# Optimization experiments

Hardware: AMD Instinct MI355X
Metric: run time of the kernel (lower is better)

Reference implementation:

```python
import jax, jax.numpy as jnp
import numpy as np

B, P, M, C = 128, 8732, 16, 3
THRESHOLD, NEG_POS_RATIO, ALPHA = 0.5, 3, 1.0


def xy_to_cxcy(xy):
    return jnp.concatenate([(xy[..., 2:] + xy[..., :2]) / 2.0, xy[..., 2:] - xy[..., :2]], axis=-1)


def cxcy_to_xy(cxcy):
    return jnp.concatenate([cxcy[..., :2] - cxcy[..., 2:] / 2.0, cxcy[..., :2] + cxcy[..., 2:] / 2.0], axis=-1)


def cxcy_to_gcxgcy(cxcy, priors_cxcy):
    return jnp.concatenate([
        (cxcy[..., :2] - priors_cxcy[..., :2]) / (priors_cxcy[..., 2:] / 10.0),
        jnp.log(cxcy[..., 2:] / priors_cxcy[..., 2:]) * 5.0], axis=-1)


def jaccard(a, b):
    # a: (M,4) xyxy, b: (P,4) xyxy -> (M,P) IoU
    lt = jnp.maximum(a[:, None, :2], b[None, :, :2])
    rb = jnp.minimum(a[:, None, 2:], b[None, :, 2:])
    wh = jnp.clip(rb - lt, 0.0)
    inter = wh[..., 0] * wh[..., 1]
    area_a = (a[:, 2] - a[:, 0]) * (a[:, 3] - a[:, 1])
    area_b = (b[:, 2] - b[:, 0]) * (b[:, 3] - b[:, 1])
    return inter / (area_a[:, None] + area_b[None, :] - inter)


def setup_inputs() -> dict:
    key = jax.random.key(0)
    k1, k2, k3, k4, k5, k6 = jax.random.split(key, 6)
    predicted_locs = jax.random.normal(k1, (B, P, 4), dtype=jnp.float32)
    predicted_scores = jax.random.normal(k2, (B, P, C), dtype=jnp.float32)
    xy = jax.random.uniform(k3, (B, M, 2), minval=0.0, maxval=0.7)
    wh = jax.random.uniform(k4, (B, M, 2), minval=0.05, maxval=0.3)
    boxes = jnp.concatenate([xy, xy + wh], axis=-1).astype(jnp.float32)
    labels = jax.random.randint(k5, (B, M), 1, 4)  # classes {1,2,3}
    pc = jax.random.uniform(k6, (P, 2), minval=0.0, maxval=1.0)
    pwh = jax.random.uniform(jax.random.fold_in(k6, 1), (P, 2), minval=0.05, maxval=0.5)
    priors_cxcy = jnp.concatenate([pc, pwh], axis=-1).astype(jnp.float32)
    return {"predicted_locs": predicted_locs, "predicted_scores": predicted_scores,
            "boxes": boxes, "labels": labels, "priors_cxcy": priors_cxcy}


def _match_one(boxes_i, labels_i, priors_xy, priors_cxcy):
    ov = jaccard(boxes_i, priors_xy)                # (M, P)
    ov_prior = ov.max(axis=0)                       # best overlap per prior
    obj_prior = ov.argmax(axis=0)                   # best object per prior
    prior_obj = ov.argmax(axis=1)                   # best prior per object
    n_obj = boxes_i.shape[0]
    obj_prior = obj_prior.at[prior_obj].set(jnp.arange(n_obj))
    ov_prior = ov_prior.at[prior_obj].set(1.0)
    lab = jnp.where(ov_prior < THRESHOLD, 0, labels_i[obj_prior])
    tl = cxcy_to_gcxgcy(xy_to_cxcy(boxes_i[obj_prior]), priors_cxcy)
    return tl, lab


def reference(predicted_locs, predicted_scores, boxes, labels, priors_cxcy):
    priors_xy = cxcy_to_xy(priors_cxcy)
    true_locs, true_classes = jax.vmap(_match_one, in_axes=(0, 0, None, None))(
        boxes, labels, priors_xy, priors_cxcy)      # (B,P,4), (B,P)
    positive = true_classes > 0                      # (B,P)
    n_pos = positive.sum(axis=1)                     # (B,)
    n_pos_total = n_pos.sum()

    # localization loss: L1Loss (mean over selected positive elements)
    l1 = jnp.abs(predicted_locs - true_locs).sum(axis=-1)   # (B,P)
    loc_loss = jnp.where(n_pos_total > 0,
                         (l1 * positive).sum() / (4.0 * jnp.maximum(n_pos_total, 1).astype(jnp.float32)),
                         0.0)

    # multi-label one-hot targets (classes 1,2,3; 3 = pair -> targets cols 1&2)
    tc = true_classes.reshape(-1)
    ignore = tc == -1
    pair = tc == 3
    target = jax.nn.one_hot(tc + 1, 5, dtype=predicted_scores.dtype)[:, 1:4]  # (B*P,3)
    target = target.at[:, 1].set(jnp.where(pair, 1.0, target[:, 1]))
    target = target.at[:, 2].set(jnp.where(pair, 1.0, target[:, 2]))

    # BCEWithLogits, summed over classes
    logits = predicted_scores.reshape(-1, C)
    bce = (jnp.logaddexp(0.0, logits) - logits * target).sum(axis=1)  # (B*P,)
    conf_all = jnp.where(ignore, 0.0, bce).reshape(true_classes.shape)  # (B,P)

    conf_pos = (conf_all * positive).sum()
    conf_neg = jnp.where(positive, 0.0, conf_all)
    conf_neg_sorted = -jnp.sort(-conf_neg, axis=1)   # descending per row
    ranks = jnp.arange(P)[None, :]
    hard_neg = ranks < (NEG_POS_RATIO * n_pos)[:, None]
    conf_hard_neg = (conf_neg_sorted * hard_neg).sum()

    conf_loss = (conf_hard_neg + conf_pos) / (1e-10 + n_pos_total.astype(jnp.float32))
    total = conf_loss + ALPHA * loc_loss
    return total, conf_loss, loc_loss, n_pos
```

## Files before the change

### kernel.cpp

```cpp
#include <hip/hip_runtime.h>
#include <hip/hip_fp16.h>
#include <cstdint>
#include <cmath>

#define B_ 128
#define P_ 8732
#define QU_ 2183
#define M_ 16
#define NT 1024
#define NW 16
#define NP9 9
#define TAIL_ (QU_ - 2*NT)

__device__ __forceinline__ float softplusf(float x) {
    float e = __builtin_amdgcn_exp2f(fabsf(x) * -1.44269504f);
    return fmaxf(x, 0.0f) + 0.69314718f * __builtin_amdgcn_logf(1.0f + e);
}

__device__ __forceinline__ float wred_sum_f(float v) {
#pragma unroll
    for (int o = 32; o > 0; o >>= 1) v += __shfl_down(v, o, 64);
    return v;
}
__device__ __forceinline__ int wred_sum_i(int v) {
#pragma unroll
    for (int o = 32; o > 0; o >>= 1) v += __shfl_down(v, o, 64);
    return v;
}

__device__ __forceinline__ void phaseD(
    int r, int p, float bv, int bm, float4 pr,
    float x0, float x1, float x2,
    const float* s_boxes, const int* s_labels,
    const float* __restrict__ plocs,
    unsigned char* __restrict__ objov, unsigned short* __restrict__ bcew,
    int& np, float& cp, float& ls)
{
    bool pos = bv >= 0.5f;
    objov[(size_t)r * P_ + p] = (unsigned char)(bm | (pos ? 0x80 : 0));
    int lab = pos ? s_labels[bm] : 0;
    float t0 = (lab == 0) ? 1.0f : 0.0f;
    float t1 = (lab == 1 || lab == 3) ? 1.0f : 0.0f;
    float t2 = (lab == 2 || lab == 3) ? 1.0f : 0.0f;
    float bce = (softplusf(x0) - x0*t0) + (softplusf(x1) - x1*t1) + (softplusf(x2) - x2*t2);
    float hb = 0.0f;
    if (pos) {
        np++; cp += bce;
        float4 bb = ((const float4*)s_boxes)[bm];
        float cx = (bb.x + bb.z) * 0.5f, cy = (bb.y + bb.w) * 0.5f;
        float w = bb.z - bb.x, hh = bb.w - bb.y;
        float g0 = (cx - pr.x) / (pr.z * 0.1f);
        float g1 = (cy - pr.y) / (pr.w * 0.1f);
        float g2 = logf(w / pr.z) * 5.0f;
        float g3 = logf(hh / pr.w) * 5.0f;
        float4 pl = ((const float4*)plocs)[(size_t)r * P_ + p];
        ls += fabsf(pl.x - g0) + fabsf(pl.y - g1) + fabsf(pl.z - g2) + fabsf(pl.w - g3);
    } else {
        hb = bce;
    }
    bcew[(size_t)r * P_ + p] = __half_as_ushort(__float2half(hb));
}

__global__ __launch_bounds__(NT) void mbox_match_kernel(
    const float* __restrict__ plocs,
    const float* __restrict__ pscores,
    const float* __restrict__ boxes,
    const int*   __restrict__ labels,
    const float* __restrict__ priors,
    unsigned char* __restrict__ objov,
    unsigned short* __restrict__ bcew,
    int2* __restrict__ cand,
    float* __restrict__ pcf, float* __restrict__ plc, int* __restrict__ pnp,
    unsigned int* __restrict__ gz)
{
    __shared__ float s_boxes[M_ * 4];
    __shared__ float s_area[M_];
    __shared__ int   s_labels[M_];
    __shared__ int2  s_cand[NW][M_];
    __shared__ float s_pf[2 * NW];
    __shared__ int   s_pi[NW];

    const int bk = blockIdx.x;
    const int r  = bk >> 2;
    const int q  = bk & 3;
    const int tid = threadIdx.x;
    const int lane = tid & 63;
    const int wid = tid >> 6;
    const int p0 = q * QU_;

    if (bk == 0 && tid < 4) gz[tid] = 0u;

    const int  pA = p0 + tid;
    const int  pB = p0 + NT + tid;
    const bool cok = tid < TAIL_;
    const int  pC = cok ? (p0 + 2 * NT + tid) : pA;

    float4 prA = ((const float4*)priors)[pA];
    float4 prB = ((const float4*)priors)[pB];
    float4 prC = ((const float4*)priors)[pC];

    const float* scA = pscores + ((size_t)r * P_ + pA) * 3;
    const float* scB = pscores + ((size_t)r * P_ + pB) * 3;
    const float* scC = pscores + ((size_t)r * P_ + pC) * 3;
    float xA0 = scA[0], xA1 = scA[1], xA2 = scA[2];
    float xB0 = scB[0], xB1 = scB[1], xB2 = scB[2];
    float xC0 = scC[0], xC1 = scC[1], xC2 = scC[2];

    if (tid < M_ * 4) s_boxes[tid] = boxes[r * M_ * 4 + tid];
    if (tid >= 64 && tid < 64 + M_) s_labels[tid - 64] = labels[r * M_ + (tid - 64)];
    __syncthreads();
    if (tid < M_) {
        float x0 = s_boxes[tid*4+0], y0 = s_boxes[tid*4+1];
        float x1 = s_boxes[tid*4+2], y1 = s_boxes[tid*4+3];
        s_area[tid] = (x1 - x0) * (y1 - y0);
    }
    __syncthreads();

    float aX0 = prA.x - prA.z*0.5f, aY0 = prA.y - prA.w*0.5f;
    float aX1 = prA.x + prA.z*0.5f, aY1 = prA.y + prA.w*0.5f;
    float aAr = prA.z * prA.w;
    float bX0 = prB.x - prB.z*0.5f, bY0 = prB.y - prB.w*0.5f;
    float bX1 = prB.x + prB.z*0.5f, bY1 = prB.y + prB.w*0.5f;
    float bAr = prB.z * prB.w;
    float cX0 = prC.x - prC.z*0.5f, cY0 = prC.y - prC.w*0.5f;
    float cX1 = prC.x + prC.z*0.5f, cY1 = prC.y + prC.w*0.5f;
    float cAr = prC.z * prC.w;

    float bvA = -1.0f, bvB = -1.0f, bvC = -1.0f;
    int   bmA = 0,     bmB = 0,     bmC = 0;

#pragma unroll
    for (int m = 0; m < M_; ++m) {
        float4 bb = ((const float4*)s_boxes)[m];
        float mar = s_area[m];

        float ltx, lty, rbx, rby, wx, wy, inter;

        ltx = fmaxf(bb.x, aX0); lty = fmaxf(bb.y, aY0);
        rbx = fminf(bb.z, aX1); rby = fminf(bb.w, aY1);
        wx = fmaxf(rbx - ltx, 0.0f); wy = fmaxf(rby - lty, 0.0f);
        inter = wx * wy;
        float ovA = inter * __builtin_amdgcn_rcpf(mar + aAr - inter);

        ltx = fmaxf(bb.x, bX0); lty = fmaxf(bb.y, bY0);
        rbx = fminf(bb.z, bX1); rby = fminf(bb.w, bY1);
        wx = fmaxf(rbx - ltx, 0.0f); wy = fmaxf(rby - lty, 0.0f);
        inter = wx * wy;
        float ovB = inter * __builtin_amdgcn_rcpf(mar + bAr - inter);

        ltx = fmaxf(bb.x, cX0); lty = fmaxf(bb.y, cY0);
        rbx = fminf(bb.z, cX1); rby = fminf(bb.w, cY1);
        wx = fmaxf(rbx - ltx, 0.0f); wy = fmaxf(rby - lty, 0.0f);
        inter = wx * wy;
        float ovC = inter * __builtin_amdgcn_rcpf(mar + cAr - inter);
        ovC = cok ? ovC : -1.0f;

        if (ovA > bvA) { bvA = ovA; bmA = m; }
        if (ovB > bvB) { bvB = ovB; bmB = m; }
        if (ovC > bvC) { bvC = ovC; bmC = m; }

        float v = ovA; int which = 0;
        if (ovB > v) { v = ovB; which = 1; }
        if (ovC > v) { v = ovC; which = 2; }
        int idx = p0 + tid + (which << 10);

#pragma unroll
        for (int o = 32; o > 0; o >>= 1) {
            float v2 = __shfl_down(v, o, 64);
            int   i2 = __shfl_down(idx, o, 64);
            if (v2 > v || (v2 == v && i2 < idx)) { v = v2; idx = i2; }
        }
        if (lane == 0) s_cand[wid][m] = make_int2(__float_as_int(v), idx);
    }

    int np = 0; float cp = 0.0f, ls = 0.0f;
    phaseD(r, pA, bvA, bmA, prA, xA0, xA1, xA2, s_boxes, s_labels,
           plocs, objov, bcew, np, cp, ls);
    phaseD(r, pB, bvB, bmB, prB, xB0, xB1, xB2, s_boxes, s_labels,
           plocs, objov, bcew, np, cp, ls);
    if (cok)
        phaseD(r, pC, bvC, bmC, prC, xC0, xC1, xC2, s_boxes, s_labels,
               plocs, objov, bcew, np, cp, ls);

    cp = wred_sum_f(cp);
    ls = wred_sum_f(ls);
    np = wred_sum_i(np);
    if (lane == 0) { s_pf[wid] = cp; s_pf[NW + wid] = ls; s_pi[wid] = np; }
    __syncthreads();

    if (tid < M_) {
        int2 c0 = s_cand[0][tid];
        float bv = __int_as_float(c0.x); int bidx = c0.y;
#pragma unroll
        for (int w = 1; w < NW; ++w) {
            int2 c = s_cand[w][tid];
            float v = __int_as_float(c.x);
            if (v > bv || (v == bv && c.y < bidx)) { bv = v; bidx = c.y; }
        }
        cand[bk * M_ + tid] = make_int2(__float_as_int(bv), bidx);
    }
    if (tid == 0) {
        float c2 = 0.0f, l2 = 0.0f; int n2 = 0;
#pragma unroll
        for (int w = 0; w < NW; ++w) { c2 += s_pf[w]; l2 += s_pf[NW + w]; n2 += s_pi[w]; }
        pcf[bk] = c2; plc[bk] = l2; pnp[bk] = n2;
    }
}

__global__ __launch_bounds__(NT) void mbox_loss_kernel(
    const float* __restrict__ plocs,
    const float* __restrict__ pscores,
    const float* __restrict__ boxes,
    const int*   __restrict__ labels,
    const float* __restrict__ priors,
    const unsigned char* __restrict__ objov,
    const unsigned short* __restrict__ bcew,
    const int2* __restrict__ cand,
    const float* __restrict__ pcf, const float* __restrict__ plc,
    const int* __restrict__ pnp,
    float* __restrict__ out,
    unsigned int* __restrict__ g_cnt,
    float* __restrict__ g_conf, float* __restrict__ g_loc, int* __restrict__ g_np)
{
    __shared__ float s_boxes[M_ * 4];
    __shared__ int   s_labels[M_];
    __shared__ int   s_po[M_];
    __shared__ float s_pf[2 * NW];
    __shared__ int   s_pi[NW];
    __shared__ int   s_cnt2[2][NW];
    __shared__ float s_scal[2];
    __shared__ int   s_npos;

    const int r = blockIdx.x;
    const int tid = threadIdx.x;
    const int lane = tid & 63;
    const int wid = tid >> 6;

    if (tid < M_ * 4) s_boxes[tid] = boxes[r * M_ * 4 + tid];
    if (tid >= 64 && tid < 64 + M_) s_labels[tid - 64] = labels[r * M_ + (tid - 64)];
    if (tid >= 128 && tid < 128 + M_) {
        int m = tid - 128;
        int2 c = cand[(r * 4) * M_ + m];
        float v = __int_as_float(c.x); int idx = c.y;
#pragma unroll
        for (int qq = 1; qq < 4; ++qq) {
            int2 c2 = cand[(r * 4 + qq) * M_ + m];
            float v2 = __int_as_float(c2.x);
            if (v2 > v) { v = v2; idx = c2.y; }
        }
        s_po[m] = idx;
    }
    __syncthreads();

    int fv_b[NP9];
#pragma unroll
    for (int i = 0; i < NP9; ++i) {
        int p = tid + i * NT;
        fv_b[i] = (p < P_) ? (int)bcew[(size_t)r * P_ + p] : 0;
    }

    if (wid == 0) {
        float dcp = 0.0f, dls = 0.0f; int dnp = 0;
        if (lane < M_) {
            const int m = lane;
            const int idx = s_po[m];
            bool owner = true;
            for (int m2 = m + 1; m2 < M_; ++m2)
                if (s_po[m2] == idx) owner = false;
            if (owner) {
                unsigned char byte = objov[(size_t)r * P_ + idx];
                bool oldpos = (byte & 0x80) != 0;
                int  oldobj = byte & 15;
                const float* sc = pscores + ((size_t)r * P_ + idx) * 3;
                float x0 = sc[0], x1 = sc[1], x2 = sc[2];
                float S = softplusf(x0) + softplusf(x1) + softplusf(x2);
                float4 pr = ((const float4*)priors)[idx];
                float4 pl = ((const float4*)plocs)[(size_t)r * P_ + idx];
                {
                    int lab = s_labels[m];
                    float t0 = (lab == 0) ? 1.0f : 0.0f;
                    float t1 = (lab == 1 || lab == 3) ? 1.0f : 0.0f;
                    float t2 = (lab == 2 || lab == 3) ? 1.0f : 0.0f;
                    dcp += S - (x0*t0 + x1*t1 + x2*t2);
                    float bx0 = s_boxes[m*4+0], by0 = s_boxes[m*4+1];
                    float bx1 = s_boxes[m*4+2], by1 = s_boxes[m*4+3];
                    float cx = (bx0+bx1)*0.5f, cy = (by0+by1)*0.5f;
                    float w = bx1-bx0, hh = by1-by0;
                    float g0 = (cx - pr.x) / (pr.z * 0.1f);
                    float g1 = (cy - pr.y) / (pr.w * 0.1f);
                    float g2 = logf(w / pr.z) * 5.0f;
                    float g3 = logf(hh / pr.w) * 5.0f;
                    dls += fabsf(pl.x-g0)+fabsf(pl.y-g1)+fabsf(pl.z-g2)+fabsf(pl.w-g3);
                    dnp += 1;
                }
                if (oldpos) {
                    int lab = s_labels[oldobj];
                    float t0 = (lab == 0) ? 1.0f : 0.0f;
                    float t1 = (lab == 1 || lab == 3) ? 1.0f : 0.0f;
                    float t2 = (lab == 2 || lab == 3) ? 1.0f : 0.0f;
                    dcp -= S - (x0*t0 + x1*t1 + x2*t2);
                    float bx0 = s_boxes[oldobj*4+0], by0 = s_boxes[oldobj*4+1];
                    float bx1 = s_boxes[oldobj*4+2], by1 = s_boxes[oldobj*4+3];
                    float cx = (bx0+bx1)*0.5f, cy = (by0+by1)*0.5f;
                    float w = bx1-bx0, hh = by1-by0;
                    float g0 = (cx - pr.x) / (pr.z * 0.1f);
                    float g1 = (cy - pr.y) / (pr.w * 0.1f);
                    float g2 = logf(w / pr.z) * 5.0f;
                    float g3 = logf(hh / pr.w) * 5.0f;
                    dls -= fabsf(pl.x-g0)+fabsf(pl.y-g1)+fabsf(pl.z-g2)+fabsf(pl.w-g3);
                    dnp -= 1;
                }
            }
        }
        dcp = wred_sum_f(dcp);
        dls = wred_sum_f(dls);
        dnp = wred_sum_i(dnp);
        if (lane == 0) {
            float cp = dcp, lsx = dls; int np = dnp;
#pragma unroll
            for (int qq = 0; qq < 4; ++qq) {
                cp  += pcf[r * 4 + qq];
                lsx += plc[r * 4 + qq];
                np  += pnp[r * 4 + qq];
            }
            s_scal[0] = cp; s_scal[1] = lsx; s_npos = np;
        }
    }
    __syncthreads();
    const int npos_row = s_npos;

#pragma unroll
    for (int i = 0; i < NP9; ++i) {
        int p = tid + i * NT;
#pragma unroll
        for (int j = 0; j < M_; ++j)
            if (s_po[j] == p) fv_b[i] = 0;
    }

    int k = 3 * npos_row;
    if (k > P_) k = P_;
    float hard_sum = 0.0f;
    if (k > 0) {
        int lo = -1, hi = 0x7C00;
        for (int it = 0; it < 15; ++it) {
            int mid = (lo + hi) >> 1;
            int c = 0;
#pragma unroll
            for (int i = 0; i < NP9; ++i) c += (fv_b[i] > mid) ? 1 : 0;
            c = wred_sum_i(c);
            if (lane == 0) s_cnt2[it & 1][wid] = c;
            __syncthreads();
            int cnt = 0;
#pragma unroll
            for (int w = 0; w < NW; ++w) cnt += s_cnt2[it & 1][w];
            if (cnt < k) hi = mid; else lo = mid;
        }
        int tb = hi;
        float tval = __half2float(__ushort_as_half((unsigned short)tb));
        float lsum = 0.0f; int lcnt = 0;
#pragma unroll
        for (int i = 0; i < NP9; ++i) {
            if (fv_b[i] > tb) {
                lsum += __half2float(__ushort_as_half((unsigned short)fv_b[i]));
                lcnt++;
            }
        }
        lsum = wred_sum_f(lsum);
        lcnt = wred_sum_i(lcnt);
        if (lane == 0) { s_pf[wid] = lsum; s_pi[wid] = lcnt; }
        __syncthreads();
        if (tid == 0) {
            float sv = 0.0f; int sc2 = 0;
#pragma unroll
            for (int w = 0; w < NW; ++w) { sv += s_pf[w]; sc2 += s_pi[w]; }
            hard_sum = sv + (float)(k - sc2) * tval;
        }
    }

    if (tid == 0) {
        float conf_row = s_scal[0] + hard_sum;
        float loc_row  = s_scal[1];
        out[3 + r] = (float)npos_row;
        atomicAdd(g_conf, conf_row);
        atomicAdd(g_loc,  loc_row);
        atomicAdd(g_np,   npos_row);
        __threadfence();
        unsigned int done = atomicAdd(g_cnt, 1u);
        if (done == B_ - 1) {
            float ct = atomicAdd(g_conf, 0.0f);
            float lt = atomicAdd(g_loc,  0.0f);
            int   np = atomicAdd(g_np,   0);
            float npt = (float)np;
            float conf_loss = ct / (1e-10f + npt);
            float loc_loss = (np > 0) ? lt / (4.0f * fmaxf(npt, 1.0f)) : 0.0f;
            out[0] = conf_loss + loc_loss;
            out[1] = conf_loss;
            out[2] = loc_loss;
        }
    }
}

extern "C" void kernel_launch(void* const* d_in, const int* in_sizes, int n_in,
                              void* d_out, int out_size, void* d_ws, size_t ws_size,
                              hipStream_t stream) {
    const float* plocs   = (const float*)d_in[0];
    const float* pscores = (const float*)d_in[1];
    const float* boxes   = (const float*)d_in[2];
    const int*   labels  = (const int*)  d_in[3];
    const float* priors  = (const float*)d_in[4];
    float* out = (float*)d_out;

    char* ws = (char*)d_ws;
    unsigned int* g_cnt  = (unsigned int*)ws;
    float*        g_conf = (float*)(ws + 4);
    float*        g_loc  = (float*)(ws + 8);
    int*          g_np   = (int*)(ws + 12);
    float*        pcf    = (float*)(ws + 64);
    float*        plc    = (float*)(ws + 2112);
    int*          pnp    = (int*)(ws + 4160);
    int2*         cand   = (int2*)(ws + 8192);
    unsigned char* objov = (unsigned char*)(ws + 73728);
    unsigned short* bcew = (unsigned short*)(ws + 73728 + (size_t)B_ * P_);

    mbox_match_kernel<<<4 * B_, NT, 0, stream>>>(plocs, pscores, boxes, labels, priors,
                                                 objov, bcew, cand, pcf, plc, pnp,
                                                 (unsigned int*)ws);
    mbox_loss_kernel<<<B_, NT, 0, stream>>>(plocs, pscores, boxes, labels, priors,
                                            objov, bcew, cand, pcf, plc, pnp,
                                            out, g_cnt, g_conf, g_loc, g_np);
}
```

Before: 136.8 us.

## Shrink loss kernel to one wavefront per row and drop objov buffer

The match kernel replaces the per-object wave shuffle argmax with packed 64-bit LDS atomicMax into four sub-slots. It no longer writes the objov byte array; the loss kernel recomputes the old best-object assignment for the few forced priors instead. The loss kernel now runs a single 64-thread wavefront per row, stages the padded fp16 BCE row into LDS, and performs the top-k bisection in 144 registers per lane with shuffle reductions only, removing block-wide barriers. The tradeoffs are 128 small blocks with low parallelism and heavy register pressure, plus LDS atomic contention in the match loop.

```diff
diff --git a/kernel.cpp b/kernel.cpp
--- a/kernel.cpp
+++ b/kernel.cpp
@@ -9,8 +9,9 @@
 #define M_ 16
 #define NT 1024
 #define NW 16
-#define NP9 9
 #define TAIL_ (QU_ - 2*NT)
+#define PSTRIDE 9216
+#define NFV 144
 
 __device__ __forceinline__ float softplusf(float x) {
     float e = __builtin_amdgcn_exp2f(fabsf(x) * -1.44269504f);
@@ -33,11 +34,10 @@
     float x0, float x1, float x2,
     const float* s_boxes, const int* s_labels,
     const float* __restrict__ plocs,
-    unsigned char* __restrict__ objov, unsigned short* __restrict__ bcew,
+    unsigned short* __restrict__ bcew,
     int& np, float& cp, float& ls)
 {
     bool pos = bv >= 0.5f;
-    objov[(size_t)r * P_ + p] = (unsigned char)(bm | (pos ? 0x80 : 0));
     int lab = pos ? s_labels[bm] : 0;
     float t0 = (lab == 0) ? 1.0f : 0.0f;
     float t1 = (lab == 1 || lab == 3) ? 1.0f : 0.0f;
@@ -58,7 +58,7 @@
     } else {
         hb = bce;
     }
-    bcew[(size_t)r * P_ + p] = __half_as_ushort(__float2half(hb));
+    bcew[(size_t)r * PSTRIDE + p] = __half_as_ushort(__float2half(hb));
 }
 
 __global__ __launch_bounds__(NT) void mbox_match_kernel(
@@ -67,7 +67,6 @@
     const float* __restrict__ boxes,
     const int*   __restrict__ labels,
     const float* __restrict__ priors,
-    unsigned char* __restrict__ objov,
     unsigned short* __restrict__ bcew,
     int2* __restrict__ cand,
     float* __restrict__ pcf, float* __restrict__ plc, int* __restrict__ pnp,
@@ -76,7 +75,7 @@
     __shared__ float s_boxes[M_ * 4];
     __shared__ float s_area[M_];
     __shared__ int   s_labels[M_];
-    __shared__ int2  s_cand[NW][M_];
+    __shared__ unsigned long long s_obj[M_ * 4];
     __shared__ float s_pf[2 * NW];
     __shared__ int   s_pi[NW];
 
@@ -91,9 +90,9 @@
     if (bk == 0 && tid < 4) gz[tid] = 0u;
 
     const int  pA = p0 + tid;
-    const int  pB = p0 + NT + tid;
+    const int  pB = pA + NT;
     const bool cok = tid < TAIL_;
-    const int  pC = cok ? (p0 + 2 * NT + tid) : pA;
+    const int  pC = cok ? (pB + NT) : pA;
 
     float4 prA = ((const float4*)priors)[pA];
     float4 prB = ((const float4*)priors)[pB];
@@ -108,6 +107,8 @@
 
     if (tid < M_ * 4) s_boxes[tid] = boxes[r * M_ * 4 + tid];
     if (tid >= 64 && tid < 64 + M_) s_labels[tid - 64] = labels[r * M_ + (tid - 64)];
+    if (tid >= 128 && tid < 128 + M_ * 4)
+        s_obj[tid - 128] = (unsigned long long)(unsigned)(16383 - p0);
     __syncthreads();
     if (tid < M_) {
         float x0 = s_boxes[tid*4+0], y0 = s_boxes[tid*4+1];
@@ -128,6 +129,7 @@
 
     float bvA = -1.0f, bvB = -1.0f, bvC = -1.0f;
     int   bmA = 0,     bmB = 0,     bmC = 0;
+    const int sub = wid & 3;
 
 #pragma unroll
     for (int m = 0; m < M_; ++m) {
@@ -148,39 +150,38 @@
         inter = wx * wy;
         float ovB = inter * __builtin_amdgcn_rcpf(mar + bAr - inter);
 
-        ltx = fmaxf(bb.x, cX0); lty = fmaxf(bb.y, cY0);
-        rbx = fminf(bb.z, cX1); rby = fminf(bb.w, cY1);
-        wx = fmaxf(rbx - ltx, 0.0f); wy = fmaxf(rby - lty, 0.0f);
-        inter = wx * wy;
-        float ovC = inter * __builtin_amdgcn_rcpf(mar + cAr - inter);
-        ovC = cok ? ovC : -1.0f;
+        float ovC = -1.0f;
+        if (cok) {
+            ltx = fmaxf(bb.x, cX0); lty = fmaxf(bb.y, cY0);
+            rbx = fminf(bb.z, cX1); rby = fminf(bb.w, cY1);
+            wx = fmaxf(rbx - ltx, 0.0f); wy = fmaxf(rby - lty, 0.0f);
+            inter = wx * wy;
+            ovC = inter * __builtin_amdgcn_rcpf(mar + cAr - inter);
+        }
 
         if (ovA > bvA) { bvA = ovA; bmA = m; }
         if (ovB > bvB) { bvB = ovB; bmB = m; }
         if (ovC > bvC) { bvC = ovC; bmC = m; }
 
-        float v = ovA; int which = 0;
-        if (ovB > v) { v = ovB; which = 1; }
-        if (ovC > v) { v = ovC; which = 2; }
-        int idx = p0 + tid + (which << 10);
-
-#pragma unroll
-        for (int o = 32; o > 0; o >>= 1) {
-            float v2 = __shfl_down(v, o, 64);
-            int   i2 = __shfl_down(idx, o, 64);
-            if (v2 > v || (v2 == v && i2 < idx)) { v = v2; idx = i2; }
-        }
-        if (lane == 0) s_cand[wid][m] = make_int2(__float_as_int(v), idx);
+        float v = ovA; int idx = pA;
+        if (ovB > v) { v = ovB; idx = pB; }
+        if (ovC > v) { v = ovC; idx = pC; }
+        if (v > 0.0f) {
+            unsigned long long pk =
+                ((unsigned long long)__float_as_uint(v) << 32)
+                | (unsigned long long)(unsigned)(16383 - idx);
+            atomicMax(&s_obj[(m << 2) | sub], pk);
+        }
     }
 
     int np = 0; float cp = 0.0f, ls = 0.0f;
     phaseD(r, pA, bvA, bmA, prA, xA0, xA1, xA2, s_boxes, s_labels,
-           plocs, objov, bcew, np, cp, ls);
+           plocs, bcew, np, cp, ls);
     phaseD(r, pB, bvB, bmB, prB, xB0, xB1, xB2, s_boxes, s_labels,
-           plocs, objov, bcew, np, cp, ls);
+           plocs, bcew, np, cp, ls);
     if (cok)
         phaseD(r, pC, bvC, bmC, prC, xC0, xC1, xC2, s_boxes, s_labels,
-               plocs, objov, bcew, np, cp, ls);
+               plocs, bcew, np, cp, ls);
 
     cp = wred_sum_f(cp);
     ls = wred_sum_f(ls);
@@ -189,15 +190,17 @@
     __syncthreads();
 
     if (tid < M_) {
-        int2 c0 = s_cand[0][tid];
-        float bv = __int_as_float(c0.x); int bidx = c0.y;
-#pragma unroll
-        for (int w = 1; w < NW; ++w) {
-            int2 c = s_cand[w][tid];
-            float v = __int_as_float(c.x);
-            if (v > bv || (v == bv && c.y < bidx)) { bv = v; bidx = c.y; }
-        }
-        cand[bk * M_ + tid] = make_int2(__float_as_int(bv), bidx);
+        unsigned long long b0 = s_obj[(tid << 2) | 0];
+        unsigned long long b1 = s_obj[(tid << 2) | 1];
+        unsigned long long b2 = s_obj[(tid << 2) | 2];
+        unsigned long long b3 = s_obj[(tid << 2) | 3];
+        unsigned long long bb = b0;
+        if (b1 > bb) bb = b1;
+        if (b2 > bb) bb = b2;
+        if (b3 > bb) bb = b3;
+        float v = __uint_as_float((unsigned)(bb >> 32));
+        int idx = 16383 - (int)(bb & 0xFFFFFFFFull);
+        cand[bk * M_ + tid] = make_int2(__float_as_int(v), idx);
     }
     if (tid == 0) {
         float c2 = 0.0f, l2 = 0.0f; int n2 = 0;
@@ -207,13 +210,12 @@
     }
 }
 
-__global__ __launch_bounds__(NT) void mbox_loss_kernel(
+__global__ __launch_bounds__(64) void mbox_loss_kernel(
     const float* __restrict__ plocs,
     const float* __restrict__ pscores,
     const float* __restrict__ boxes,
     const int*   __restrict__ labels,
     const float* __restrict__ priors,
-    const unsigned char* __restrict__ objov,
     const unsigned short* __restrict__ bcew,
     const int2* __restrict__ cand,
     const float* __restrict__ pcf, const float* __restrict__ plc,
@@ -222,119 +224,131 @@
     unsigned int* __restrict__ g_cnt,
     float* __restrict__ g_conf, float* __restrict__ g_loc, int* __restrict__ g_np)
 {
+    __shared__ unsigned short s_fv[PSTRIDE];
     __shared__ float s_boxes[M_ * 4];
     __shared__ int   s_labels[M_];
     __shared__ int   s_po[M_];
-    __shared__ float s_pf[2 * NW];
-    __shared__ int   s_pi[NW];
-    __shared__ int   s_cnt2[2][NW];
-    __shared__ float s_scal[2];
-    __shared__ int   s_npos;
 
     const int r = blockIdx.x;
-    const int tid = threadIdx.x;
-    const int lane = tid & 63;
-    const int wid = tid >> 6;
-
-    if (tid < M_ * 4) s_boxes[tid] = boxes[r * M_ * 4 + tid];
-    if (tid >= 64 && tid < 64 + M_) s_labels[tid - 64] = labels[r * M_ + (tid - 64)];
-    if (tid >= 128 && tid < 128 + M_) {
-        int m = tid - 128;
-        int2 c = cand[(r * 4) * M_ + m];
+    const int lane = threadIdx.x;
+
+    {
+        const uint4* src = (const uint4*)(bcew + (size_t)r * PSTRIDE);
+        uint4* dst = (uint4*)s_fv;
+#pragma unroll
+        for (int j = 0; j < 18; ++j)
+            dst[j * 64 + lane] = src[j * 64 + lane];
+    }
+    s_boxes[lane] = boxes[r * 64 + lane];
+    if (lane < M_) s_labels[lane] = labels[r * M_ + lane];
+    if (lane < M_) {
+        int2 c = cand[(r * 4) * M_ + lane];
         float v = __int_as_float(c.x); int idx = c.y;
 #pragma unroll
         for (int qq = 1; qq < 4; ++qq) {
-            int2 c2 = cand[(r * 4 + qq) * M_ + m];
+            int2 c2 = cand[(r * 4 + qq) * M_ + lane];
             float v2 = __int_as_float(c2.x);
             if (v2 > v) { v = v2; idx = c2.y; }
         }
-        s_po[m] = idx;
+        s_po[lane] = idx;
     }
     __syncthreads();
 
-    int fv_b[NP9];
-#pragma unroll
-    for (int i = 0; i < NP9; ++i) {
-        int p = tid + i * NT;
-        fv_b[i] = (p < P_) ? (int)bcew[(size_t)r * P_ + p] : 0;
-    }
-
-    if (wid == 0) {
-        float dcp = 0.0f, dls = 0.0f; int dnp = 0;
-        if (lane < M_) {
-            const int m = lane;
-            const int idx = s_po[m];
-            bool owner = true;
-            for (int m2 = m + 1; m2 < M_; ++m2)
-                if (s_po[m2] == idx) owner = false;
-            if (owner) {
-                unsigned char byte = objov[(size_t)r * P_ + idx];
-                bool oldpos = (byte & 0x80) != 0;
-                int  oldobj = byte & 15;
-                const float* sc = pscores + ((size_t)r * P_ + idx) * 3;
-                float x0 = sc[0], x1 = sc[1], x2 = sc[2];
-                float S = softplusf(x0) + softplusf(x1) + softplusf(x2);
-                float4 pr = ((const float4*)priors)[idx];
-                float4 pl = ((const float4*)plocs)[(size_t)r * P_ + idx];
-                {
-                    int lab = s_labels[m];
-                    float t0 = (lab == 0) ? 1.0f : 0.0f;
-                    float t1 = (lab == 1 || lab == 3) ? 1.0f : 0.0f;
-                    float t2 = (lab == 2 || lab == 3) ? 1.0f : 0.0f;
-                    dcp += S - (x0*t0 + x1*t1 + x2*t2);
-                    float bx0 = s_boxes[m*4+0], by0 = s_boxes[m*4+1];
-                    float bx1 = s_boxes[m*4+2], by1 = s_boxes[m*4+3];
-                    float cx = (bx0+bx1)*0.5f, cy = (by0+by1)*0.5f;
-                    float w = bx1-bx0, hh = by1-by0;
-                    float g0 = (cx - pr.x) / (pr.z * 0.1f);
-                    float g1 = (cy - pr.y) / (pr.w * 0.1f);
-                    float g2 = logf(w / pr.z) * 5.0f;
-                    float g3 = logf(hh / pr.w) * 5.0f;
-                    dls += fabsf(pl.x-g0)+fabsf(pl.y-g1)+fabsf(pl.z-g2)+fabsf(pl.w-g3);
-                    dnp += 1;
-                }
-                if (oldpos) {
-                    int lab = s_labels[oldobj];
-                    float t0 = (lab == 0) ? 1.0f : 0.0f;
-                    float t1 = (lab == 1 || lab == 3) ? 1.0f : 0.0f;
-                    float t2 = (lab == 2 || lab == 3) ? 1.0f : 0.0f;
-                    dcp -= S - (x0*t0 + x1*t1 + x2*t2);
-                    float bx0 = s_boxes[oldobj*4+0], by0 = s_boxes[oldobj*4+1];
-                    float bx1 = s_boxes[oldobj*4+2], by1 = s_boxes[oldobj*4+3];
-                    float cx = (bx0+bx1)*0.5f, cy = (by0+by1)*0.5f;
-                    float w = bx1-bx0, hh = by1-by0;
-                    float g0 = (cx - pr.x) / (pr.z * 0.1f);
-                    float g1 = (cy - pr.y) / (pr.w * 0.1f);
-                    float g2 = logf(w / pr.z) * 5.0f;
-                    float g3 = logf(hh / pr.w) * 5.0f;
-                    dls -= fabsf(pl.x-g0)+fabsf(pl.y-g1)+fabsf(pl.z-g2)+fabsf(pl.w-g3);
-                    dnp -= 1;
-                }
+    for (int p = P_ + lane; p < PSTRIDE; p += 64) s_fv[p] = 0;
+    if (lane < M_) s_fv[s_po[lane]] = 0;
+
+    float dcp = 0.0f, dls = 0.0f; int dnp = 0;
+    if (lane < M_) {
+        const int m = lane;
+        const int idx = s_po[m];
+        bool owner = true;
+        for (int m2 = m + 1; m2 < M_; ++m2)
+            if (s_po[m2] == idx) owner = false;
+        if (owner) {
+            float4 pr = ((const float4*)priors)[idx];
+            float pX0 = pr.x - pr.z*0.5f, pY0 = pr.y - pr.w*0.5f;
+            float pX1 = pr.x + pr.z*0.5f, pY1 = pr.y + pr.w*0.5f;
+            float pAr = pr.z * pr.w;
+            float obv = -1.0f; int obm = 0;
+#pragma unroll
+            for (int mm = 0; mm < M_; ++mm) {
+                float4 bb = ((const float4*)s_boxes)[mm];
+                float mar = (bb.z - bb.x) * (bb.w - bb.y);
+                float ltx = fmaxf(bb.x, pX0), lty = fmaxf(bb.y, pY0);
+                float rbx = fminf(bb.z, pX1), rby = fminf(bb.w, pY1);
+                float wx = fmaxf(rbx - ltx, 0.0f), wy = fmaxf(rby - lty, 0.0f);
+                float inter = wx * wy;
+                float ov = inter * __builtin_amdgcn_rcpf(mar + pAr - inter);
+                if (ov > obv) { obv = ov; obm = mm; }
             }
-        }
-        dcp = wred_sum_f(dcp);
-        dls = wred_sum_f(dls);
-        dnp = wred_sum_i(dnp);
-        if (lane == 0) {
-            float cp = dcp, lsx = dls; int np = dnp;
-#pragma unroll
-            for (int qq = 0; qq < 4; ++qq) {
-                cp  += pcf[r * 4 + qq];
-                lsx += plc[r * 4 + qq];
-                np  += pnp[r * 4 + qq];
+            bool oldpos = obv >= 0.5f;
+            int  oldobj = obm;
+
+            const float* sc = pscores + ((size_t)r * P_ + idx) * 3;
+            float x0 = sc[0], x1 = sc[1], x2 = sc[2];
+            float S = softplusf(x0) + softplusf(x1) + softplusf(x2);
+            float4 pl = ((const float4*)plocs)[(size_t)r * P_ + idx];
+            {
+                int lab = s_labels[m];
+                float t0 = (lab == 0) ? 1.0f : 0.0f;
+                float t1 = (lab == 1 || lab == 3) ? 1.0f : 0.0f;
+                float t2 = (lab == 2 || lab == 3) ? 1.0f : 0.0f;
+                dcp += S - (x0*t0 + x1*t1 + x2*t2);
+                float bx0 = s_boxes[m*4+0], by0 = s_boxes[m*4+1];
+                float bx1 = s_boxes[m*4+2], by1 = s_boxes[m*4+3];
+                float cx = (bx0+bx1)*0.5f, cy = (by0+by1)*0.5f;
+                float w = bx1-bx0, hh = by1-by0;
+                float g0 = (cx - pr.x) / (pr.z * 0.1f);
+                float g1 = (cy - pr.y) / (pr.w * 0.1f);
+                float g2 = logf(w / pr.z) * 5.0f;
+                float g3 = logf(hh / pr.w) * 5.0f;
+                dls += fabsf(pl.x-g0)+fabsf(pl.y-g1)+fabsf(pl.z-g2)+fabsf(pl.w-g3);
+                dnp += 1;
             }
-            s_scal[0] = cp; s_scal[1] = lsx; s_npos = np;
-        }
-    }
+            if (oldpos) {
+                int lab = s_labels[oldobj];
+                float t0 = (lab == 0) ? 1.0f : 0.0f;
+                float t1 = (lab == 1 || lab == 3) ? 1.0f : 0.0f;
+                float t2 = (lab == 2 || lab == 3) ? 1.0f : 0.0f;
+                dcp -= S - (x0*t0 + x1*t1 + x2*t2);
+                float bx0 = s_boxes[oldobj*4+0], by0 = s_boxes[oldobj*4+1];
+                float bx1 = s_boxes[oldobj*4+2], by1 = s_boxes[oldobj*4+3];
+                float cx = (bx0+bx1)*0.5f, cy = (by0+by1)*0.5f;
+                float w = bx1-bx0, hh = by1-by0;
+                float g0 = (cx - pr.x) / (pr.z * 0.1f);
+                float g1 = (cy - pr.y) / (pr.w * 0.1f);
+                float g2 = logf(w / pr.z) * 5.0f;
+                float g3 = logf(hh / pr.w) * 5.0f;
+                dls -= fabsf(pl.x-g0)+fabsf(pl.y-g1)+fabsf(pl.z-g2)+fabsf(pl.w-g3);
+                dnp -= 1;
+            }
+        }
+    }
+    dcp = wred_sum_f(dcp);
+    dls = wred_sum_f(dls);
+    dnp = wred_sum_i(dnp);
+    float cp = 0.0f, lsx = 0.0f; int np = 0;
+    if (lane == 0) {
+        cp = dcp; lsx = dls; np = dnp;
+#pragma unroll
+        for (int qq = 0; qq < 4; ++qq) {
+            cp  += pcf[r * 4 + qq];
+            lsx += plc[r * 4 + qq];
+            np  += pnp[r * 4 + qq];
+        }
+    }
+    const int npos_row = __shfl(np, 0, 64);
+
     __syncthreads();
-    const int npos_row = s_npos;
-
-#pragma unroll
-    for (int i = 0; i < NP9; ++i) {
-        int p = tid + i * NT;
-#pragma unroll
-        for (int j = 0; j < M_; ++j)
-            if (s_po[j] == p) fv_b[i] = 0;
+
+    int fv[NFV];
+#pragma unroll
+    for (int j = 0; j < 18; ++j) {
+        uint4 d = ((const uint4*)s_fv)[j * 64 + lane];
+        fv[j*8+0] = (int)(d.x & 0xFFFFu); fv[j*8+1] = (int)(d.x >> 16);
+        fv[j*8+2] = (int)(d.y & 0xFFFFu); fv[j*8+3] = (int)(d.y >> 16);
+        fv[j*8+4] = (int)(d.z & 0xFFFFu); fv[j*8+5] = (int)(d.z >> 16);
+        fv[j*8+6] = (int)(d.w & 0xFFFFu); fv[j*8+7] = (int)(d.w >> 16);
     }
 
     int k = 3 * npos_row;
@@ -346,40 +360,29 @@
             int mid = (lo + hi) >> 1;
             int c = 0;
 #pragma unroll
-            for (int i = 0; i < NP9; ++i) c += (fv_b[i] > mid) ? 1 : 0;
-            c = wred_sum_i(c);
-            if (lane == 0) s_cnt2[it & 1][wid] = c;
-            __syncthreads();
-            int cnt = 0;
-#pragma unroll
-            for (int w = 0; w < NW; ++w) cnt += s_cnt2[it & 1][w];
-            if (cnt < k) hi = mid; else lo = mid;
+            for (int i = 0; i < NFV; ++i) c += (fv[i] > mid) ? 1 : 0;
+#pragma unroll
+            for (int o = 32; o > 0; o >>= 1) c += __shfl_xor(c, o, 64);
+            if (c < k) hi = mid; else lo = mid;
         }
         int tb = hi;
         float tval = __half2float(__ushort_as_half((unsigned short)tb));
         float lsum = 0.0f; int lcnt = 0;
 #pragma unroll
-        for (int i = 0; i < NP9; ++i) {
-            if (fv_b[i] > tb) {
-                lsum += __half2float(__ushort_as_half((unsigned short)fv_b[i]));
+        for (int i = 0; i < NFV; ++i) {
+            if (fv[i] > tb) {
+                lsum += __half2float(__ushort_as_half((unsigned short)fv[i]));
                 lcnt++;
             }
         }
         lsum = wred_sum_f(lsum);
         lcnt = wred_sum_i(lcnt);
-        if (lane == 0) { s_pf[wid] = lsum; s_pi[wid] = lcnt; }
-        __syncthreads();
-        if (tid == 0) {
-            float sv = 0.0f; int sc2 = 0;
-#pragma unroll
-            for (int w = 0; w < NW; ++w) { sv += s_pf[w]; sc2 += s_pi[w]; }
-            hard_sum = sv + (float)(k - sc2) * tval;
-        }
-    }
-
-    if (tid == 0) {
-        float conf_row = s_scal[0] + hard_sum;
-        float loc_row  = s_scal[1];
+        if (lane == 0) hard_sum = lsum + (float)(k - lcnt) * tval;
+    }
+
+    if (lane == 0) {
+        float conf_row = cp + hard_sum;
+        float loc_row  = lsx;
         out[3 + r] = (float)npos_row;
         atomicAdd(g_conf, conf_row);
         atomicAdd(g_loc,  loc_row);
@@ -389,10 +392,10 @@
         if (done == B_ - 1) {
             float ct = atomicAdd(g_conf, 0.0f);
             float lt = atomicAdd(g_loc,  0.0f);
-            int   np = atomicAdd(g_np,   0);
-            float npt = (float)np;
+            int   npt_i = atomicAdd(g_np, 0);
+            float npt = (float)npt_i;
             float conf_loss = ct / (1e-10f + npt);
-            float loc_loss = (np > 0) ? lt / (4.0f * fmaxf(npt, 1.0f)) : 0.0f;
+            float loc_loss = (npt_i > 0) ? lt / (4.0f * fmaxf(npt, 1.0f)) : 0.0f;
             out[0] = conf_loss + loc_loss;
             out[1] = conf_loss;
             out[2] = loc_loss;
@@ -419,13 +422,12 @@
     float*        plc    = (float*)(ws + 2112);
     int*          pnp    = (int*)(ws + 4160);
     int2*         cand   = (int2*)(ws + 8192);
-    unsigned char* objov = (unsigned char*)(ws + 73728);
-    unsigned short* bcew = (unsigned short*)(ws + 73728 + (size_t)B_ * P_);
+    unsigned short* bcew = (unsigned short*)(ws + 73728);
 
     mbox_match_kernel<<<4 * B_, NT, 0, stream>>>(plocs, pscores, boxes, labels, priors,
-                                                 objov, bcew, cand, pcf, plc, pnp,
+                                                 bcew, cand, pcf, plc, pnp,
                                                  (unsigned int*)ws);
-    mbox_loss_kernel<<<B_, NT, 0, stream>>>(plocs, pscores, boxes, labels, priors,
-                                            objov, bcew, cand, pcf, plc, pnp,
+    mbox_loss_kernel<<<B_, 64, 0, stream>>>(plocs, pscores, boxes, labels, priors,
+                                            bcew, cand, pcf, plc, pnp,
                                             out, g_cnt, g_conf, g_loc, g_np);
 }
```

Measured after the change: 130.8 us. -4.4%, faster.
